# Kernel optimization log

Hardware: AMD Instinct MI355X
Metric: run time of the kernel (lower is better)

## Reference

```python
import jax, jax.numpy as jnp
import numpy as np

IN_FEATURES = 64
MLP_HIDDEN = 512
LSTM_HIDDEN = 256
OUT_FEATURES = 8


def _build_tree():
    # binary-reduction tree: 100k leaves, each level halves; parent of child j at
    # level l-1 is node (j mod sizes[l]) at level l -> ~2 children per parent.
    sizes = []
    s = 100000
    while s >= 1:
        sizes.append(s)
        s //= 2
    offsets = np.cumsum([0] + sizes[:-1])
    node_order = np.concatenate([np.full(sz, l, dtype=np.int64) for l, sz in enumerate(sizes)])
    pa, ch, eo = [], [], []
    for l in range(1, len(sizes)):
        idx = np.arange(sizes[l - 1], dtype=np.int64)
        ch.append(offsets[l - 1] + idx)
        pa.append(offsets[l] + (idx % sizes[l]))
        eo.append(np.full(sizes[l - 1], l, dtype=np.int64))
    adjacency_list = np.stack([np.concatenate(pa), np.concatenate(ch)], axis=1)
    return node_order, adjacency_list, np.concatenate(eo), len(sizes)


def _linear_params(key, fan_in, fan_out):
    k1, k2 = jax.random.split(key)
    lim = 1.0 / np.sqrt(fan_in)
    w = jax.random.uniform(k1, (fan_in, fan_out), jnp.float32, -lim, lim)
    b = jax.random.uniform(k2, (fan_out,), jnp.float32, -lim, lim)
    return w, b


def setup_inputs() -> dict:
    key = jax.random.key(0)
    node_order, adjacency_list, edge_order, num_levels = _build_tree()
    n = node_order.shape[0]
    ks = jax.random.split(key, 10)
    features = jax.random.normal(ks[0], (n, IN_FEATURES), jnp.float32)
    enc_w1, enc_b1 = _linear_params(ks[1], IN_FEATURES, MLP_HIDDEN)
    enc_w2, enc_b2 = _linear_params(ks[2], MLP_HIDDEN, MLP_HIDDEN // 2)
    enc_w3, enc_b3 = _linear_params(ks[3], MLP_HIDDEN // 2, MLP_HIDDEN // 4)
    enc_w4, enc_b4 = _linear_params(ks[4], MLP_HIDDEN // 4, MLP_HIDDEN // 8)
    w_iou, b_iou = _linear_params(ks[5], MLP_HIDDEN // 8, 3 * LSTM_HIDDEN)
    u_iou, _ = _linear_params(ks[6], LSTM_HIDDEN, 3 * LSTM_HIDDEN)
    w_f, b_f = _linear_params(ks[7], MLP_HIDDEN // 8, LSTM_HIDDEN)
    u_f, _ = _linear_params(ks[8], LSTM_HIDDEN, LSTM_HIDDEN)
    cls_w, cls_b = _linear_params(ks[9], LSTM_HIDDEN, OUT_FEATURES)
    return {
        "features": features,
        "node_order": jnp.asarray(node_order),
        "adjacency_list": jnp.asarray(adjacency_list),
        "edge_order": jnp.asarray(edge_order),
        "num_levels": num_levels,
        "enc_w1": enc_w1, "enc_b1": enc_b1, "enc_w2": enc_w2, "enc_b2": enc_b2,
        "enc_w3": enc_w3, "enc_b3": enc_b3, "enc_w4": enc_w4, "enc_b4": enc_b4,
        "w_iou": w_iou, "b_iou": b_iou, "u_iou": u_iou,
        "w_f": w_f, "b_f": b_f, "u_f": u_f,
        "cls_w": cls_w, "cls_b": cls_b,
    }


def _forward(features, node_order, adjacency_list, edge_order, num_levels,
             enc_w1, enc_b1, enc_w2, enc_b2, enc_w3, enc_b3, enc_w4, enc_b4,
             w_iou, b_iou, u_iou, w_f, b_f, u_f, cls_w, cls_b):
    x = features
    for w, b in ((enc_w1, enc_b1), (enc_w2, enc_b2), (enc_w3, enc_b3), (enc_w4, enc_b4)):
        x = jax.nn.relu(x @ w + b)
    n = x.shape[0]
    hdim = u_f.shape[0]
    parents = adjacency_list[:, 0]
    children = adjacency_list[:, 1]
    wx_iou = x @ w_iou + b_iou  # [N, 3H], precomputed once for all levels
    wx_f = x @ w_f + b_f        # [N, H]

    def step(carry, level):
        h, c = carry
        nmask = (node_order == level)[:, None]                    # [N,1]
        emask = (edge_order == level)[:, None].astype(x.dtype)    # [E,1]
        child_h = h[children]                                     # [E,H]
        child_c = c[children]                                     # [E,H]
        # child-sum of hidden states per parent (only this level's edges)
        h_sum = jax.ops.segment_sum(child_h * emask, parents, num_segments=n)
        # per-edge forget gate, scatter f*c to parents
        f = jax.nn.sigmoid(wx_f[parents] + child_h @ u_f)
        c_sum = jax.ops.segment_sum(f * child_c * emask, parents, num_segments=n)
        iou = wx_iou + h_sum @ u_iou                               # U_iou has no bias -> zero for leaves
        i, o, u = jnp.split(iou, 3, axis=1)
        c_new = jnp.where(nmask, jax.nn.sigmoid(i) * jnp.tanh(u) + c_sum, c)
        h_new = jnp.where(nmask, jax.nn.sigmoid(o) * jnp.tanh(c_new), h)
        return (h_new, c_new), None

    zero = jnp.zeros((n, hdim), x.dtype)
    (h, _), _ = jax.lax.scan(step, (zero, zero), jnp.arange(num_levels))
    return jax.nn.softmax(h @ cls_w + cls_b, axis=1)


def reference(features, node_order, adjacency_list, edge_order, num_levels,
              enc_w1, enc_b1, enc_w2, enc_b2, enc_w3, enc_b3, enc_w4, enc_b4,
              w_iou, b_iou, u_iou, w_f, b_f, u_f, cls_w, cls_b):
    return _forward(features, node_order, adjacency_list, edge_order, num_levels,
                    enc_w1, enc_b1, enc_w2, enc_b2, enc_w3, enc_b3, enc_w4, enc_b4,
                    w_iou, b_iou, u_iou, w_f, b_f, u_f, cls_w, cls_b)
```

## Files before the change

### kernel.cpp

```cpp
#include <hip/hip_runtime.h>
#include <math.h>


typedef __attribute__((ext_vector_type(8))) short bf16x8;
typedef __attribute__((ext_vector_type(4))) float f32x4;

__device__ __forceinline__ float sigm(float x)  { return 1.0f / (1.0f + __expf(-x)); }
__device__ __forceinline__ float tanhx(float x) { return 1.0f - 2.0f / (__expf(2.0f * x) + 1.0f); }

__device__ __forceinline__ float b2f(unsigned short u) {
    union { unsigned int i; float f; } v; v.i = ((unsigned int)u) << 16; return v.f;
}
__device__ __forceinline__ unsigned short f2b(float f) {
    union { float f; unsigned int i; } v; v.f = f;
    unsigned int r = v.i + 0x7FFFu + ((v.i >> 16) & 1u);
    return (unsigned short)(r >> 16);
}


__device__ __forceinline__ void stage_a_bf16(unsigned short* dst,
        const unsigned short* src, int srcStride, int validRows, int tid) {
    const int row = tid >> 2, ch = (tid & 3) << 3;
    bf16x8 v = {0, 0, 0, 0, 0, 0, 0, 0};
    if (row < validRows)
        v = *(const bf16x8*)&src[(size_t)row * srcStride + ch];
    *(bf16x8*)&dst[row * 32 + ch] = v;
}

__device__ __forceinline__ void stage_a_fp32(unsigned short* dst,
        const float* src, int srcStride, int validRows, int tid) {
    const int row = tid >> 2, ch = (tid & 3) << 3;
    bf16x8 v = {0, 0, 0, 0, 0, 0, 0, 0};
    if (row < validRows) {
        const float4 a = *(const float4*)&src[(size_t)row * srcStride + ch];
        const float4 b = *(const float4*)&src[(size_t)row * srcStride + ch + 4];
        v[0] = (short)f2b(a.x); v[1] = (short)f2b(a.y);
        v[2] = (short)f2b(a.z); v[3] = (short)f2b(a.w);
        v[4] = (short)f2b(b.x); v[5] = (short)f2b(b.y);
        v[6] = (short)f2b(b.z); v[7] = (short)f2b(b.w);
    }
    *(bf16x8*)&dst[row * 32 + ch] = v;
}

__device__ __forceinline__ void stage_b64(unsigned short* dst,
        const unsigned short* src, int K, int tid) {
    const int row = tid >> 2, ch = (tid & 3) << 3;
    *(bf16x8*)&dst[row * 32 + ch] = *(const bf16x8*)&src[(size_t)row * K + ch];
}

__device__ __forceinline__ void stage_b192(unsigned short* dst,
        const unsigned short* Wt, int n0, int K, int k0, int tid) {
    const int row = tid >> 2, ch = (tid & 3) << 3;
#pragma unroll
    for (int g = 0; g < 3; ++g)
        *(bf16x8*)&dst[(g * 64 + row) * 32 + ch] =
            *(const bf16x8*)&Wt[(size_t)(g * 256 + n0 + row) * K + k0 + ch];
}

__device__ __forceinline__ bf16x8 frag(const unsigned short* lds, int rowBase, int lane) {
    return *(const bf16x8*)&lds[(rowBase + (lane & 15)) * 32 + ((lane >> 4) << 3)];
}

__global__ __launch_bounds__(256) void tpose_bf16(const float* __restrict__ W,
        unsigned short* __restrict__ Wt, int K, int N) {
    const int idx = blockIdx.x * 256 + threadIdx.x;
    if (idx < K * N) {
        const int nn = idx / K, kk = idx - nn * K;
        Wt[idx] = f2b(W[(size_t)kk * N + nn]);
    }
}

template<int AFP32>
__global__ __launch_bounds__(256) void mgemm(
    const void* __restrict__ Av, const unsigned short* __restrict__ Wt,
    const float* __restrict__ bias, unsigned short* __restrict__ Cb,
    int M, int N, int K)
{
    __shared__ unsigned short As[64 * 32];
    __shared__ unsigned short Bs[64 * 32];
    const int tid = threadIdx.x, lane = tid & 63, wave = tid >> 6;
    const int m0 = blockIdx.x * 64, n0 = blockIdx.y * 64;
    const int mr = wave * 16, fr = lane & 15, fq = lane >> 4;
    const f32x4 z = {0.f, 0.f, 0.f, 0.f};
    f32x4 acc[4] = {z, z, z, z};

    for (int k0 = 0; k0 < K; k0 += 32) {
        if (AFP32)
            stage_a_fp32(As, (const float*)Av + (size_t)m0 * K + k0, K, M - m0, tid);
        else
            stage_a_bf16(As, (const unsigned short*)Av + (size_t)m0 * K + k0, K, M - m0, tid);
        stage_b64(Bs, Wt + (size_t)n0 * K + k0, K, tid);
        __syncthreads();
        const bf16x8 a = frag(As, mr, lane);
#pragma unroll
        for (int ns = 0; ns < 4; ++ns)
            acc[ns] = __builtin_amdgcn_mfma_f32_16x16x32_bf16(a, frag(Bs, ns * 16, lane), acc[ns], 0, 0, 0);
        __syncthreads();
    }
#pragma unroll
    for (int ns = 0; ns < 4; ++ns)
#pragma unroll
        for (int i = 0; i < 4; ++i) {
            const int m = m0 + mr + fq * 4 + i;
            if (m < M) {
                const int nn = n0 + ns * 16 + fr;
                Cb[(size_t)m * N + nn] = f2b(fmaxf(acc[ns][i] + bias[nn], 0.f));
            }
        }
}

template<int LEAF>
__global__ __launch_bounds__(256) void level_mfma(
    const unsigned short* __restrict__ x4b, int offP,
    const unsigned short* __restrict__ h_prev, const unsigned short* __restrict__ c_prev,
    const unsigned short* __restrict__ Wt_iou, const unsigned short* __restrict__ Wt_uiou,
    const float* __restrict__ b_iou,
    const unsigned short* __restrict__ Wt_f, const unsigned short* __restrict__ Wt_uf,
    const float* __restrict__ b_f,
    unsigned short* __restrict__ h_cur, unsigned short* __restrict__ c_cur,
    int P, int C)
{
    __shared__ unsigned short As[64 * 32];
    __shared__ unsigned short Bs[192 * 32];
    const int tid = threadIdx.x, lane = tid & 63, wave = tid >> 6;
    const int m0 = blockIdx.x * 64, n0 = blockIdx.y * 64;
    const int mr = wave * 16, fr = lane & 15, fq = lane >> 4;
    const f32x4 z = {0.f, 0.f, 0.f, 0.f};
    const int nch = (!LEAF && m0 == 0 && C > 2 * P) ? 3 : 2;

    f32x4 cs[4] = {z, z, z, z};

    if (!LEAF) {
        f32x4 cm[4] = {z, z, z, z};
        for (int k0 = 0; k0 < 64; k0 += 32) {
            stage_a_bf16(As, x4b + (size_t)(offP + m0) * 64 + k0, 64, P - m0, tid);
            stage_b64(Bs, Wt_f + (size_t)n0 * 64 + k0, 64, tid);
            __syncthreads();
            const bf16x8 a = frag(As, mr, lane);
#pragma unroll
            for (int ns = 0; ns < 4; ++ns)
                cm[ns] = __builtin_amdgcn_mfma_f32_16x16x32_bf16(a, frag(Bs, ns * 16, lane), cm[ns], 0, 0, 0);
            __syncthreads();
        }
        for (int t = 0; t < nch; ++t) {
            f32x4 fa[4] = {z, z, z, z};
            const int base = t * P + m0;
            for (int k0 = 0; k0 < 256; k0 += 32) {
                stage_a_bf16(As, h_prev + (size_t)base * 256 + k0, 256, C - base, tid);
                stage_b64(Bs, Wt_uf + (size_t)n0 * 256 + k0, 256, tid);
                __syncthreads();
                const bf16x8 a = frag(As, mr, lane);
#pragma unroll
                for (int ns = 0; ns < 4; ++ns)
                    fa[ns] = __builtin_amdgcn_mfma_f32_16x16x32_bf16(a, frag(Bs, ns * 16, lane), fa[ns], 0, 0, 0);
                __syncthreads();
            }
#pragma unroll
            for (int ns = 0; ns < 4; ++ns)
#pragma unroll
                for (int i = 0; i < 4; ++i) {
                    const int m = m0 + mr + fq * 4 + i;
                    const int crow = t * P + m;
                    if (m < P && crow < C) {
                        const int nn = n0 + ns * 16 + fr;
                        const float fv = sigm(fa[ns][i] + cm[ns][i] + b_f[nn]);
                        cs[ns][i] += fv * b2f(c_prev[(size_t)crow * 256 + nn]);
                    }
                }
        }
    }

    f32x4 io[3][4] = {{z, z, z, z}, {z, z, z, z}, {z, z, z, z}};
    for (int k0 = 0; k0 < 64; k0 += 32) {
        stage_a_bf16(As, x4b + (size_t)(offP + m0) * 64 + k0, 64, P - m0, tid);
        stage_b192(Bs, Wt_iou, n0, 64, k0, tid);
        __syncthreads();
        const bf16x8 a = frag(As, mr, lane);
#pragma unroll
        for (int g = 0; g < 3; ++g)
#pragma unroll
            for (int ns = 0; ns < 4; ++ns)
                io[g][ns] = __builtin_amdgcn_mfma_f32_16x16x32_bf16(a, frag(Bs, g * 64 + ns * 16, lane), io[g][ns], 0, 0, 0);
        __syncthreads();
    }
    if (!LEAF) {
        for (int t = 0; t < nch; ++t) {
            const int base = t * P + m0;
            for (int k0 = 0; k0 < 256; k0 += 32) {
                stage_a_bf16(As, h_prev + (size_t)base * 256 + k0, 256, C - base, tid);
                stage_b192(Bs, Wt_uiou, n0, 256, k0, tid);
                __syncthreads();
                const bf16x8 a = frag(As, mr, lane);
#pragma unroll
                for (int g = 0; g < 3; ++g)
#pragma unroll
                    for (int ns = 0; ns < 4; ++ns)
                        io[g][ns] = __builtin_amdgcn_mfma_f32_16x16x32_bf16(a, frag(Bs, g * 64 + ns * 16, lane), io[g][ns], 0, 0, 0);
                __syncthreads();
            }
        }
    }

#pragma unroll
    for (int ns = 0; ns < 4; ++ns)
#pragma unroll
        for (int i = 0; i < 4; ++i) {
            const int m = m0 + mr + fq * 4 + i;
            if (m < P) {
                const int nn = n0 + ns * 16 + fr;
                const float iv = io[0][ns][i] + b_iou[nn];
                const float ov = io[1][ns][i] + b_iou[256 + nn];
                const float uv = io[2][ns][i] + b_iou[512 + nn];
                const float cv = sigm(iv) * tanhx(uv) + cs[ns][i];
                c_cur[(size_t)m * 256 + nn] = f2b(cv);
                h_cur[(size_t)m * 256 + nn] = f2b(sigm(ov) * tanhx(cv));
            }
        }
}

__global__ __launch_bounds__(256) void cls_kernel(
    const unsigned short* __restrict__ h, const float* __restrict__ cls_w,
    const float* __restrict__ cls_b, float* __restrict__ out, int P)
{
    __shared__ float hs[32][257];
    __shared__ float wsm[256 * 8];
    __shared__ float bs[8];
    const int tid = threadIdx.x;
    const int row0 = blockIdx.x * 32;
    for (int i = tid; i < 2048; i += 256) wsm[i] = cls_w[i];
    if (tid < 8) bs[tid] = cls_b[tid];
    for (int it = 0; it < 32; ++it) {
        const int row = row0 + it;
        hs[it][tid] = (row < P) ? b2f(h[(size_t)row * 256 + tid]) : 0.f;
    }
    __syncthreads();
    const int r = tid >> 3, j = tid & 7;
    float acc = bs[j];
#pragma unroll 4
    for (int k = 0; k < 256; ++k) acc += hs[r][k] * wsm[k * 8 + j];
    float mx = acc;
    for (int off = 1; off < 8; off <<= 1) mx = fmaxf(mx, __shfl_xor(mx, off, 8));
    const float e = __expf(acc - mx);
    float s = e;
    for (int off = 1; off < 8; off <<= 1) s += __shfl_xor(s, off, 8);
    const int row = row0 + r;
    if (row < P) out[(size_t)row * 8 + j] = e / s;
}

extern "C" void kernel_launch(void* const* d_in, const int* in_sizes, int n_in,
                              void* d_out, int out_size, void* d_ws, size_t ws_size,
                              hipStream_t stream)
{
    (void)n_in; (void)out_size; (void)ws_size;
    const float* features = (const float*)d_in[0];
    const float* enc_w1 = (const float*)d_in[5];
    const float* enc_b1 = (const float*)d_in[6];
    const float* enc_w2 = (const float*)d_in[7];
    const float* enc_b2 = (const float*)d_in[8];
    const float* enc_w3 = (const float*)d_in[9];
    const float* enc_b3 = (const float*)d_in[10];
    const float* enc_w4 = (const float*)d_in[11];
    const float* enc_b4 = (const float*)d_in[12];
    const float* w_iou  = (const float*)d_in[13];
    const float* b_iou  = (const float*)d_in[14];
    const float* u_iou  = (const float*)d_in[15];
    const float* w_f    = (const float*)d_in[16];
    const float* b_f    = (const float*)d_in[17];
    const float* u_f    = (const float*)d_in[18];
    const float* cls_w  = (const float*)d_in[19];
    const float* cls_b  = (const float*)d_in[20];
    float* out = (float*)d_out;

    const int n = in_sizes[0] / 64;

    int sz[32], nl = 0;
    for (int s = 100000; s >= 1; s /= 2) sz[nl++] = s;
    int off[33];
    off[0] = 0;
    for (int i = 0; i < nl; ++i) off[i + 1] = off[i] + sz[i];

    unsigned short* wsb = (unsigned short*)d_ws;
    unsigned short* Wt_e1   = wsb;
    unsigned short* Wt_e2   = Wt_e1 + 32768;
    unsigned short* Wt_e3   = Wt_e2 + 131072;
    unsigned short* Wt_e4   = Wt_e3 + 32768;
    unsigned short* Wt_iou  = Wt_e4 + 8192;
    unsigned short* Wt_uiou = Wt_iou + 49152;
    unsigned short* Wt_f    = Wt_uiou + 196608;
    unsigned short* Wt_uf   = Wt_f + 16384;
    unsigned short* x4b     = Wt_uf + 65536;
    unsigned short* hA      = x4b + (size_t)n * 64;
    unsigned short* hB      = hA + (size_t)100000 * 256;
    unsigned short* cA      = hB + (size_t)50000 * 256;
    unsigned short* cB      = cA + (size_t)100000 * 256;
    unsigned short* hbuf[2] = {hA, hB};
    unsigned short* cbuf[2] = {cA, cB};

    tpose_bf16<<<(64 * 512 + 255) / 256, 256, 0, stream>>>(enc_w1, Wt_e1, 64, 512);
    tpose_bf16<<<(512 * 256 + 255) / 256, 256, 0, stream>>>(enc_w2, Wt_e2, 512, 256);
    tpose_bf16<<<(256 * 128 + 255) / 256, 256, 0, stream>>>(enc_w3, Wt_e3, 256, 128);
    tpose_bf16<<<(128 * 64 + 255) / 256, 256, 0, stream>>>(enc_w4, Wt_e4, 128, 64);
    tpose_bf16<<<(64 * 768 + 255) / 256, 256, 0, stream>>>(w_iou, Wt_iou, 64, 768);
    tpose_bf16<<<(256 * 768 + 255) / 256, 256, 0, stream>>>(u_iou, Wt_uiou, 256, 768);
    tpose_bf16<<<(64 * 256 + 255) / 256, 256, 0, stream>>>(w_f, Wt_f, 64, 256);
    tpose_bf16<<<(256 * 256 + 255) / 256, 256, 0, stream>>>(u_f, Wt_uf, 256, 256);

    const int CR = 50000;
    unsigned short* t1b = hA;
    unsigned short* t2b = hB;
    unsigned short* t3b = cA;
    for (int ch = 0; ch * CR < n; ++ch) {
        const int r0 = ch * CR;
        const int M = (n - r0 < CR) ? (n - r0) : CR;
        mgemm<1><<<dim3((M + 63) / 64, 8), 256, 0, stream>>>(
            features + (size_t)r0 * 64, Wt_e1, enc_b1, t1b, M, 512, 64);
        mgemm<0><<<dim3((M + 63) / 64, 4), 256, 0, stream>>>(
            t1b, Wt_e2, enc_b2, t2b, M, 256, 512);
        mgemm<0><<<dim3((M + 63) / 64, 2), 256, 0, stream>>>(
            t2b, Wt_e3, enc_b3, t3b, M, 128, 256);
        mgemm<0><<<dim3((M + 63) / 64, 1), 256, 0, stream>>>(
            t3b, Wt_e4, enc_b4, x4b + (size_t)r0 * 64, M, 64, 128);
    }

    {
        const int P = sz[0];
        level_mfma<1><<<dim3((P + 63) / 64, 4), 256, 0, stream>>>(
            x4b, 0, (const unsigned short*)nullptr, (const unsigned short*)nullptr,
            Wt_iou, Wt_uiou, b_iou, Wt_f, Wt_uf, b_f, hA, cA, P, 0);
        cls_kernel<<<dim3((P + 31) / 32), 256, 0, stream>>>(hA, cls_w, cls_b, out, P);
    }

    for (int l = 1; l < nl; ++l) {
        const int P = sz[l], C = sz[l - 1];
        unsigned short* hp = hbuf[(l - 1) & 1]; unsigned short* cp = cbuf[(l - 1) & 1];
        unsigned short* hc = hbuf[l & 1];       unsigned short* cc = cbuf[l & 1];
        level_mfma<0><<<dim3((P + 63) / 64, 4), 256, 0, stream>>>(
            x4b, off[l], hp, cp, Wt_iou, Wt_uiou, b_iou, Wt_f, Wt_uf, b_f,
            hc, cc, P, C);
        cls_kernel<<<dim3((P + 31) / 32), 256, 0, stream>>>(
            hc, cls_w, cls_b, out + (size_t)off[l] * 8, P);
    }
}
```

Before: 1.724 ms.

## Pad LDS rows, widen encoder GEMM N-tiles, fuse forget and iou passes

Pads the LDS row stride from 32 to 40 bf16 elements to cut bank conflicts on fragment reads. Each encoder GEMM block now covers the whole N dimension or a 256-wide slice, so the A tile is staged once and reused across more MFMA columns. In the level kernel the forget-gate and iou GEMMs share a single pass over x4 and h_prev, so the children's hidden rows are staged once instead of twice. This adds LDS use and accumulator registers, which may lower occupancy, and the encoder grids have fewer blocks.

```diff
diff --git a/kernel.cpp b/kernel.cpp
--- a/kernel.cpp
+++ b/kernel.cpp
@@ -4,6 +4,8 @@
 
 typedef __attribute__((ext_vector_type(8))) short bf16x8;
 typedef __attribute__((ext_vector_type(4))) float f32x4;
+
+#define LDP 40
 
 __device__ __forceinline__ float sigm(float x)  { return 1.0f / (1.0f + __expf(-x)); }
 __device__ __forceinline__ float tanhx(float x) { return 1.0f - 2.0f / (__expf(2.0f * x) + 1.0f); }
@@ -24,7 +26,7 @@
     bf16x8 v = {0, 0, 0, 0, 0, 0, 0, 0};
     if (row < validRows)
         v = *(const bf16x8*)&src[(size_t)row * srcStride + ch];
-    *(bf16x8*)&dst[row * 32 + ch] = v;
+    *(bf16x8*)&dst[row * LDP + ch] = v;
 }
 
 __device__ __forceinline__ void stage_a_fp32(unsigned short* dst,
@@ -39,26 +41,31 @@
         v[4] = (short)f2b(b.x); v[5] = (short)f2b(b.y);
         v[6] = (short)f2b(b.z); v[7] = (short)f2b(b.w);
     }
-    *(bf16x8*)&dst[row * 32 + ch] = v;
-}
-
-__device__ __forceinline__ void stage_b64(unsigned short* dst,
-        const unsigned short* src, int K, int tid) {
+    *(bf16x8*)&dst[row * LDP + ch] = v;
+}
+
+__device__ __forceinline__ void stage_b_fiou(unsigned short* dst,
+        const unsigned short* Wf, const unsigned short* Wiou,
+        int n0, int K, int k0, int tid) {
     const int row = tid >> 2, ch = (tid & 3) << 3;
-    *(bf16x8*)&dst[row * 32 + ch] = *(const bf16x8*)&src[(size_t)row * K + ch];
-}
-
-__device__ __forceinline__ void stage_b192(unsigned short* dst,
-        const unsigned short* Wt, int n0, int K, int k0, int tid) {
+    *(bf16x8*)&dst[row * LDP + ch] =
+        *(const bf16x8*)&Wf[(size_t)(n0 + row) * K + k0 + ch];
+#pragma unroll
+    for (int g = 0; g < 3; ++g)
+        *(bf16x8*)&dst[(64 + g * 64 + row) * LDP + ch] =
+            *(const bf16x8*)&Wiou[(size_t)(g * 256 + n0 + row) * K + k0 + ch];
+}
+
+__device__ __forceinline__ void stage_b_sub(unsigned short* dst,
+        const unsigned short* Wt, int n0, int K, int k0, int nsub, int tid) {
     const int row = tid >> 2, ch = (tid & 3) << 3;
-#pragma unroll
-    for (int g = 0; g < 3; ++g)
-        *(bf16x8*)&dst[(g * 64 + row) * 32 + ch] =
-            *(const bf16x8*)&Wt[(size_t)(g * 256 + n0 + row) * K + k0 + ch];
+    for (int s = 0; s < nsub; ++s)
+        *(bf16x8*)&dst[(s * 64 + row) * LDP + ch] =
+            *(const bf16x8*)&Wt[(size_t)(n0 + s * 64 + row) * K + k0 + ch];
 }
 
 __device__ __forceinline__ bf16x8 frag(const unsigned short* lds, int rowBase, int lane) {
-    return *(const bf16x8*)&lds[(rowBase + (lane & 15)) * 32 + ((lane >> 4) << 3)];
+    return *(const bf16x8*)&lds[(rowBase + (lane & 15)) * LDP + ((lane >> 4) << 3)];
 }
 
 __global__ __launch_bounds__(256) void tpose_bf16(const float* __restrict__ W,
@@ -70,41 +77,43 @@
     }
 }
 
-template<int AFP32>
+template<int NSUB, int AFP32>
 __global__ __launch_bounds__(256) void mgemm(
     const void* __restrict__ Av, const unsigned short* __restrict__ Wt,
     const float* __restrict__ bias, unsigned short* __restrict__ Cb,
     int M, int N, int K)
 {
-    __shared__ unsigned short As[64 * 32];
-    __shared__ unsigned short Bs[64 * 32];
+    __shared__ unsigned short As[64 * LDP];
+    __shared__ unsigned short Bs[NSUB * 64 * LDP];
     const int tid = threadIdx.x, lane = tid & 63, wave = tid >> 6;
-    const int m0 = blockIdx.x * 64, n0 = blockIdx.y * 64;
+    const int m0 = blockIdx.x * 64, n0 = blockIdx.y * (NSUB * 64);
     const int mr = wave * 16, fr = lane & 15, fq = lane >> 4;
     const f32x4 z = {0.f, 0.f, 0.f, 0.f};
-    f32x4 acc[4] = {z, z, z, z};
+    f32x4 acc[NSUB * 4];
+#pragma unroll
+    for (int j = 0; j < NSUB * 4; ++j) acc[j] = z;
 
     for (int k0 = 0; k0 < K; k0 += 32) {
         if (AFP32)
             stage_a_fp32(As, (const float*)Av + (size_t)m0 * K + k0, K, M - m0, tid);
         else
             stage_a_bf16(As, (const unsigned short*)Av + (size_t)m0 * K + k0, K, M - m0, tid);
-        stage_b64(Bs, Wt + (size_t)n0 * K + k0, K, tid);
+        stage_b_sub(Bs, Wt, n0, K, k0, NSUB, tid);
         __syncthreads();
         const bf16x8 a = frag(As, mr, lane);
 #pragma unroll
-        for (int ns = 0; ns < 4; ++ns)
-            acc[ns] = __builtin_amdgcn_mfma_f32_16x16x32_bf16(a, frag(Bs, ns * 16, lane), acc[ns], 0, 0, 0);
+        for (int j = 0; j < NSUB * 4; ++j)
+            acc[j] = __builtin_amdgcn_mfma_f32_16x16x32_bf16(a, frag(Bs, j * 16, lane), acc[j], 0, 0, 0);
         __syncthreads();
     }
 #pragma unroll
-    for (int ns = 0; ns < 4; ++ns)
+    for (int j = 0; j < NSUB * 4; ++j)
 #pragma unroll
         for (int i = 0; i < 4; ++i) {
             const int m = m0 + mr + fq * 4 + i;
             if (m < M) {
-                const int nn = n0 + ns * 16 + fr;
-                Cb[(size_t)m * N + nn] = f2b(fmaxf(acc[ns][i] + bias[nn], 0.f));
+                const int nn = n0 + j * 16 + fr;
+                Cb[(size_t)m * N + nn] = f2b(fmaxf(acc[j][i] + bias[nn], 0.f));
             }
         }
 }
@@ -120,39 +129,53 @@
     unsigned short* __restrict__ h_cur, unsigned short* __restrict__ c_cur,
     int P, int C)
 {
-    __shared__ unsigned short As[64 * 32];
-    __shared__ unsigned short Bs[192 * 32];
+    __shared__ unsigned short As[64 * LDP];
+    __shared__ unsigned short Bs[256 * LDP];
     const int tid = threadIdx.x, lane = tid & 63, wave = tid >> 6;
     const int m0 = blockIdx.x * 64, n0 = blockIdx.y * 64;
     const int mr = wave * 16, fr = lane & 15, fq = lane >> 4;
     const f32x4 z = {0.f, 0.f, 0.f, 0.f};
     const int nch = (!LEAF && m0 == 0 && C > 2 * P) ? 3 : 2;
 
+    f32x4 cm[4] = {z, z, z, z};
     f32x4 cs[4] = {z, z, z, z};
-
-    if (!LEAF) {
-        f32x4 cm[4] = {z, z, z, z};
-        for (int k0 = 0; k0 < 64; k0 += 32) {
-            stage_a_bf16(As, x4b + (size_t)(offP + m0) * 64 + k0, 64, P - m0, tid);
-            stage_b64(Bs, Wt_f + (size_t)n0 * 64 + k0, 64, tid);
-            __syncthreads();
-            const bf16x8 a = frag(As, mr, lane);
+    f32x4 io[3][4] = {{z, z, z, z}, {z, z, z, z}, {z, z, z, z}};
+
+    for (int k0 = 0; k0 < 64; k0 += 32) {
+        stage_a_bf16(As, x4b + (size_t)(offP + m0) * 64 + k0, 64, P - m0, tid);
+        stage_b_fiou(Bs, Wt_f, Wt_iou, n0, 64, k0, tid);
+        __syncthreads();
+        const bf16x8 a = frag(As, mr, lane);
+        if (!LEAF) {
 #pragma unroll
             for (int ns = 0; ns < 4; ++ns)
                 cm[ns] = __builtin_amdgcn_mfma_f32_16x16x32_bf16(a, frag(Bs, ns * 16, lane), cm[ns], 0, 0, 0);
-            __syncthreads();
         }
+#pragma unroll
+        for (int g = 0; g < 3; ++g)
+#pragma unroll
+            for (int ns = 0; ns < 4; ++ns)
+                io[g][ns] = __builtin_amdgcn_mfma_f32_16x16x32_bf16(a, frag(Bs, 64 + g * 64 + ns * 16, lane), io[g][ns], 0, 0, 0);
+        __syncthreads();
+    }
+
+    if (!LEAF) {
         for (int t = 0; t < nch; ++t) {
             f32x4 fa[4] = {z, z, z, z};
             const int base = t * P + m0;
             for (int k0 = 0; k0 < 256; k0 += 32) {
                 stage_a_bf16(As, h_prev + (size_t)base * 256 + k0, 256, C - base, tid);
-                stage_b64(Bs, Wt_uf + (size_t)n0 * 256 + k0, 256, tid);
+                stage_b_fiou(Bs, Wt_uf, Wt_uiou, n0, 256, k0, tid);
                 __syncthreads();
                 const bf16x8 a = frag(As, mr, lane);
 #pragma unroll
                 for (int ns = 0; ns < 4; ++ns)
                     fa[ns] = __builtin_amdgcn_mfma_f32_16x16x32_bf16(a, frag(Bs, ns * 16, lane), fa[ns], 0, 0, 0);
+#pragma unroll
+                for (int g = 0; g < 3; ++g)
+#pragma unroll
+                    for (int ns = 0; ns < 4; ++ns)
+                        io[g][ns] = __builtin_amdgcn_mfma_f32_16x16x32_bf16(a, frag(Bs, 64 + g * 64 + ns * 16, lane), io[g][ns], 0, 0, 0);
                 __syncthreads();
             }
 #pragma unroll
@@ -167,37 +190,6 @@
                         cs[ns][i] += fv * b2f(c_prev[(size_t)crow * 256 + nn]);
                     }
                 }
-        }
-    }
-
-    f32x4 io[3][4] = {{z, z, z, z}, {z, z, z, z}, {z, z, z, z}};
-    for (int k0 = 0; k0 < 64; k0 += 32) {
-        stage_a_bf16(As, x4b + (size_t)(offP + m0) * 64 + k0, 64, P - m0, tid);
-        stage_b192(Bs, Wt_iou, n0, 64, k0, tid);
-        __syncthreads();
-        const bf16x8 a = frag(As, mr, lane);
-#pragma unroll
-        for (int g = 0; g < 3; ++g)
-#pragma unroll
-            for (int ns = 0; ns < 4; ++ns)
-                io[g][ns] = __builtin_amdgcn_mfma_f32_16x16x32_bf16(a, frag(Bs, g * 64 + ns * 16, lane), io[g][ns], 0, 0, 0);
-        __syncthreads();
-    }
-    if (!LEAF) {
-        for (int t = 0; t < nch; ++t) {
-            const int base = t * P + m0;
-            for (int k0 = 0; k0 < 256; k0 += 32) {
-                stage_a_bf16(As, h_prev + (size_t)base * 256 + k0, 256, C - base, tid);
-                stage_b192(Bs, Wt_uiou, n0, 256, k0, tid);
-                __syncthreads();
-                const bf16x8 a = frag(As, mr, lane);
-#pragma unroll
-                for (int g = 0; g < 3; ++g)
-#pragma unroll
-                    for (int ns = 0; ns < 4; ++ns)
-                        io[g][ns] = __builtin_amdgcn_mfma_f32_16x16x32_bf16(a, frag(Bs, g * 64 + ns * 16, lane), io[g][ns], 0, 0, 0);
-                __syncthreads();
-            }
         }
     }
 
@@ -312,13 +304,13 @@
     for (int ch = 0; ch * CR < n; ++ch) {
         const int r0 = ch * CR;
         const int M = (n - r0 < CR) ? (n - r0) : CR;
-        mgemm<1><<<dim3((M + 63) / 64, 8), 256, 0, stream>>>(
+        mgemm<4, 1><<<dim3((M + 63) / 64, 2), 256, 0, stream>>>(
             features + (size_t)r0 * 64, Wt_e1, enc_b1, t1b, M, 512, 64);
-        mgemm<0><<<dim3((M + 63) / 64, 4), 256, 0, stream>>>(
+        mgemm<4, 0><<<dim3((M + 63) / 64, 1), 256, 0, stream>>>(
             t1b, Wt_e2, enc_b2, t2b, M, 256, 512);
-        mgemm<0><<<dim3((M + 63) / 64, 2), 256, 0, stream>>>(
+        mgemm<2, 0><<<dim3((M + 63) / 64, 1), 256, 0, stream>>>(
             t2b, Wt_e3, enc_b3, t3b, M, 128, 256);
-        mgemm<0><<<dim3((M + 63) / 64, 1), 256, 0, stream>>>(
+        mgemm<1, 0><<<dim3((M + 63) / 64, 1), 256, 0, stream>>>(
             t3b, Wt_e4, enc_b4, x4b + (size_t)r0 * 64, M, 64, 128);
     }
 
```

Result: slower. 2.024 ms (+17.4%).
